# Performance work log

Measured on AMD Instinct MI355X. Metric: run time of the kernel, lower is better.

## Reference

```python
import jax, jax.numpy as jnp
import numpy as np

PLACEHOLDER = -1
B, S, V = 128, 8, 32000  # batch, spec tokens per request, vocab
T = B * S


def setup_inputs() -> dict:
    key = jax.random.key(0)
    ks = jax.random.split(key, 8)
    target_logits = jax.random.normal(ks[0], (T, V), dtype=jnp.float32)
    dp = jax.random.uniform(ks[1], (T, V), dtype=jnp.float32)
    draft_probs = dp / jnp.sum(dp, axis=-1, keepdims=True)  # valid prob dist per token
    draft_token_ids = jax.random.randint(ks[2], (T,), 0, V, dtype=jnp.int32)
    bonus_token_ids = jax.random.randint(ks[3], (B,), 0, V, dtype=jnp.int32)
    temperature = 0.5 + jax.random.uniform(ks[4], (B,), dtype=jnp.float32)  # >0 => all random
    uniform_probs = jax.random.uniform(ks[5], (T,), dtype=jnp.float32)
    # q ~ Exponential(1), as torch's q.exponential_()
    u = jax.random.uniform(ks[6], (B, V), dtype=jnp.float32, minval=1e-10, maxval=1.0)
    q = -jnp.log(u)
    cu_num_draft_tokens = (jnp.arange(B, dtype=jnp.int32) + 1) * S
    return {
        'target_logits': target_logits,
        'draft_probs': draft_probs,
        'draft_token_ids': draft_token_ids,
        'bonus_token_ids': bonus_token_ids,
        'temperature': temperature,
        'uniform_probs': uniform_probs,
        'q': q,
        'cu_num_draft_tokens': cu_num_draft_tokens,
    }


def reference(target_logits, draft_probs, draft_token_ids, bonus_token_ids,
              temperature, uniform_probs, q, cu_num_draft_tokens):
    # compute_probs: softmax of logits / per-token expanded temperature
    temp_tok = jnp.repeat(temperature, S)  # [T]
    target_probs = jax.nn.softmax(target_logits / temp_tok[:, None], axis=-1)  # [T, V]

    tok = jnp.arange(T)
    req = tok // S  # request index per token (uniform raggedness)

    # accept/reject: target_prob/draft_prob >= u  (guard draft_prob > 0)
    p_tgt = target_probs[tok, draft_token_ids]  # [T]
    p_drf = draft_probs[tok, draft_token_ids]   # [T]
    accept = (p_drf > 0) & (p_tgt >= uniform_probs * p_drf)  # [T]

    # recovered tokens: argmax(max(p_tgt - p_drf, 0) / q) over vocab (Gumbel-max trick)
    resid = jnp.maximum(target_probs - draft_probs, 0.0)  # [T, V]
    recovered = jnp.argmax(resid / q[req], axis=-1).astype(jnp.int32)  # [T]

    # sequential accept until first rejection, then placeholder; bonus if all accepted
    accept_b = accept.reshape(B, S)
    alive = jnp.concatenate(
        [jnp.ones((B, 1), dtype=bool),
         jnp.cumprod(accept_b[:, :-1].astype(jnp.int32), axis=1).astype(bool)],
        axis=1)  # alive[b, p] = all accepts before pos p
    tok_out = jnp.where(accept_b, draft_token_ids.reshape(B, S), recovered.reshape(B, S))
    main = jnp.where(alive, tok_out, PLACEHOLDER)  # [B, S]
    all_acc = jnp.all(accept_b, axis=1)
    bonus_col = jnp.where(all_acc, bonus_token_ids, PLACEHOLDER)  # [B]
    output_token_ids = jnp.concatenate([main, bonus_col[:, None]], axis=1)  # [B, S+1]
    return output_token_ids
```

## Files before the change

kernel.cpp:

```cpp
#include <hip/hip_runtime.h>


constexpr int PLACEHOLDER = -1;
constexpr int B = 128;
constexpr int S = 8;
constexpr int V = 32000;
constexpr int T = B * S;
constexpr int NV4 = V / 4;
constexpr int CHUNKS = 4;
constexpr int CV4 = NV4 / CHUNKS;
constexpr int K2T = 512;

extern "C" __device__ float __builtin_amdgcn_exp2f(float);
extern "C" __device__ float __builtin_amdgcn_rcpf(float);

__global__ __launch_bounds__(512)
void k1_sum(const float* __restrict__ logits,
            const float* __restrict__ dprobs,
            const int*   __restrict__ draft_ids,
            const float* __restrict__ temperature,
            const float* __restrict__ uniform_probs,
            float* __restrict__ w_D,
            int*   __restrict__ w_acc)
{
    const int t   = blockIdx.x;
    const int tid = threadIdx.x, lane = tid & 63, wid = tid >> 6;
    __shared__ float s_red[8];

    const float c = 1.4426950408889634f / temperature[t >> 3];
    const float4* lrow = (const float4*)(logits + (size_t)t * V);

    int dt = 0; float l_d = 0.f, d_d = 0.f, u = 0.f;
    if (tid == 0) {
        dt  = draft_ids[t];
        l_d = logits[(size_t)t * V + dt];
        d_d = dprobs[(size_t)t * V + dt];
        u   = uniform_probs[t];
    }

    float lsum = 0.f;
    #pragma unroll 4
    for (int j = 0; j < 16; ++j) {
        const int i4 = j * 512 + tid;
        if (i4 < NV4) {
            const float4 v = lrow[i4];
            lsum += (__builtin_amdgcn_exp2f(v.x * c) +
                     __builtin_amdgcn_exp2f(v.y * c)) +
                    (__builtin_amdgcn_exp2f(v.z * c) +
                     __builtin_amdgcn_exp2f(v.w * c));
        }
    }
    #pragma unroll
    for (int off = 32; off >= 1; off >>= 1)
        lsum += __shfl_xor(lsum, off, 64);
    if (lane == 0) s_red[wid] = lsum;
    __syncthreads();
    if (tid == 0) {
        const float D = ((s_red[0] + s_red[1]) + (s_red[2] + s_red[3])) +
                        ((s_red[4] + s_red[5]) + (s_red[6] + s_red[7]));
        w_D[t] = D;
        const float e_d = __builtin_amdgcn_exp2f(l_d * c);
        w_acc[t] = (d_d > 0.f) && (e_d >= u * d_d * D);
    }
}

__global__ __launch_bounds__(K2T)
void k2_arg(const float* __restrict__ logits,
            const float* __restrict__ dprobs,
            const float* __restrict__ q,
            const float* __restrict__ temperature,
            const float* __restrict__ w_D,
            const int*   __restrict__ w_acc,
            float* __restrict__ w_bv,
            int*   __restrict__ w_bi)
{
    const int bid = blockIdx.x;
    const int b = bid >> 2, k = bid & 3;
    const int tid = threadIdx.x, lane = tid & 63, wid = tid >> 6;
    __shared__ float s_val[8];
    __shared__ int   s_idx[8];
    __shared__ int   s_needp;

    if (tid == 0) {
        int np = S;
        #pragma unroll
        for (int p = S - 1; p >= 0; --p)
            if (!w_acc[b * S + p]) np = p;
        s_needp = np;
    }
    __syncthreads();
    const int need_p = s_needp;
    if (need_p >= S) return;

    const int   t = b * S + need_p;
    const float c = 1.4426950408889634f / temperature[b];
    const float D = w_D[t];

    const float4* lrow = (const float4*)(logits + (size_t)t * V) + k * CV4;
    const float4* drow = (const float4*)(dprobs + (size_t)t * V) + k * CV4;
    const float4* qrow = (const float4*)(q      + (size_t)b * V) + k * CV4;

    float4 lv[4], dv[4], qv[4];
    #pragma unroll
    for (int j = 0; j < 4; ++j) {
        const int i = j * K2T + tid;
        if (i < CV4) lv[j] = lrow[i];
    }
    #pragma unroll
    for (int j = 0; j < 4; ++j) {
        const int i = j * K2T + tid;
        if (i < CV4) dv[j] = drow[i];
    }
    #pragma unroll
    for (int j = 0; j < 4; ++j) {
        const int i = j * K2T + tid;
        if (i < CV4) qv[j] = qrow[i];
    }

    float bestv = -__builtin_inff();
    int   besti = 0x7fffffff;

#define RS_COMP(LC, DC, QC, GIDX)                                          \
    {                                                                      \
        const float e  = __builtin_amdgcn_exp2f((LC) * c);                 \
        const float rq = __builtin_amdgcn_rcpf(QC);                        \
        const float r  = fmaf(-((DC) * rq), D, e * rq);                    \
        if (r > bestv) { bestv = r; besti = (GIDX); }                      \
    }

    #pragma unroll
    for (int j = 0; j < 4; ++j) {
        const int i = j * K2T + tid;
        if (i < CV4) {
            const int base = (k * CV4 + i) * 4;
            RS_COMP(lv[j].x, dv[j].x, qv[j].x, base + 0)
            RS_COMP(lv[j].y, dv[j].y, qv[j].y, base + 1)
            RS_COMP(lv[j].z, dv[j].z, qv[j].z, base + 2)
            RS_COMP(lv[j].w, dv[j].w, qv[j].w, base + 3)
        }
    }
#undef RS_COMP

    #pragma unroll
    for (int off = 32; off >= 1; off >>= 1) {
        const float ov = __shfl_xor(bestv, off, 64);
        const int   oi = __shfl_xor(besti, off, 64);
        if (ov > bestv || (ov == bestv && oi < besti)) { bestv = ov; besti = oi; }
    }
    if (lane == 0) { s_val[wid] = bestv; s_idx[wid] = besti; }
    __syncthreads();
    if (tid == 0) {
        float bv = s_val[0]; int bi = s_idx[0];
        #pragma unroll
        for (int w = 1; w < 8; ++w) {
            const float ov = s_val[w]; const int oi = s_idx[w];
            if (ov > bv || (ov == bv && oi < bi)) { bv = ov; bi = oi; }
        }
        w_bv[bid] = bv;
        w_bi[bid] = bi;
    }
}

__global__ __launch_bounds__(128)
void k3_fin(const int*   __restrict__ w_acc,
            const int*   __restrict__ draft_ids,
            const int*   __restrict__ bonus_ids,
            const float* __restrict__ w_bv,
            const int*   __restrict__ w_bi,
            int* __restrict__ out)
{
    const int b = threadIdx.x;
    if (b >= B) return;
    int np = S;
    #pragma unroll
    for (int p = S - 1; p >= 0; --p)
        if (!w_acc[b * S + p]) np = p;

    int rec = PLACEHOLDER;
    if (np < S) {
        float bv = -__builtin_inff(); int bi = 0x7fffffff;
        #pragma unroll
        for (int kk = 0; kk < CHUNKS; ++kk) {
            const float ov = w_bv[b * CHUNKS + kk];
            const int   oi = w_bi[b * CHUNKS + kk];
            if (ov > bv || (ov == bv && oi < bi)) { bv = ov; bi = oi; }
        }
        rec = bi;
    }

    #pragma unroll
    for (int p = 0; p < S; ++p) {
        int tok = PLACEHOLDER;
        if (p < np)       tok = draft_ids[b * S + p];
        else if (p == np) tok = rec;
        out[b * (S + 1) + p] = tok;
    }
    out[b * (S + 1) + S] = (np == S) ? bonus_ids[b] : PLACEHOLDER;
}

extern "C" void kernel_launch(void* const* d_in, const int* in_sizes, int n_in,
                              void* d_out, int out_size, void* d_ws, size_t ws_size,
                              hipStream_t stream) {
    const float* logits      = (const float*)d_in[0];
    const float* dprobs      = (const float*)d_in[1];
    const int*   draft_ids   = (const int*)d_in[2];
    const int*   bonus_ids   = (const int*)d_in[3];
    const float* temperature = (const float*)d_in[4];
    const float* uniform     = (const float*)d_in[5];
    const float* q           = (const float*)d_in[6];

    int* out = (int*)d_out;
    float* w_D   = (float*)d_ws;
    int*   w_acc = (int*)(w_D + T);
    float* w_bv  = (float*)(w_acc + T);
    int*   w_bi  = (int*)(w_bv + B * CHUNKS);

    k1_sum<<<T, 512, 0, stream>>>(logits, dprobs, draft_ids, temperature,
                                  uniform, w_D, w_acc);
    k2_arg<<<B * CHUNKS, K2T, 0, stream>>>(logits, dprobs, q, temperature,
                                           w_D, w_acc, w_bv, w_bi);
    k3_fin<<<1, 128, 0, stream>>>(w_acc, draft_ids, bonus_ids, w_bv, w_bi, out);
}
```

Measured before the change: 37.81 us.

## Fuse final output kernel into argmax kernel via atomic max and last-block finalize

Removes the third kernel by having each argmax chunk block atomically merge a packed (ordered-float value, inverted index) key into a per-request 64-bit slot. A per-request counter picks the last finishing block, which writes the output row. Requests whose drafts are all accepted write their row directly. This saves a kernel launch and a small serial tail, but adds a hipMemsetAsync on the workspace plus atomic traffic.

After: 41.76 us. 10.4% more time.

```diff
diff --git a/kernel.cpp b/kernel.cpp
--- a/kernel.cpp
+++ b/kernel.cpp
@@ -64,6 +64,11 @@
     }
 }
 
+__device__ __forceinline__ unsigned int enc_f32(float f) {
+    const unsigned int s = __float_as_uint(f);
+    return ((int)s >= 0) ? (s | 0x80000000u) : ~s;
+}
+
 __global__ __launch_bounds__(K2T)
 void k2_arg(const float* __restrict__ logits,
             const float* __restrict__ dprobs,
@@ -71,8 +76,11 @@
             const float* __restrict__ temperature,
             const float* __restrict__ w_D,
             const int*   __restrict__ w_acc,
-            float* __restrict__ w_bv,
-            int*   __restrict__ w_bi)
+            const int*   __restrict__ draft_ids,
+            const int*   __restrict__ bonus_ids,
+            unsigned long long* __restrict__ w_best,
+            int* __restrict__ w_cnt,
+            int* __restrict__ out)
 {
     const int bid = blockIdx.x;
     const int b = bid >> 2, k = bid & 3;
@@ -90,7 +98,15 @@
     }
     __syncthreads();
     const int need_p = s_needp;
-    if (need_p >= S) return;
+    if (need_p >= S) {
+        if (k == 0 && tid == 0) {
+            #pragma unroll
+            for (int p = 0; p < S; ++p)
+                out[b * (S + 1) + p] = draft_ids[b * S + p];
+            out[b * (S + 1) + S] = bonus_ids[b];
+        }
+        return;
+    }
 
     const int   t = b * S + need_p;
     const float c = 1.4426950408889634f / temperature[b];
@@ -156,46 +172,29 @@
             const float ov = s_val[w]; const int oi = s_idx[w];
             if (ov > bv || (ov == bv && oi < bi)) { bv = ov; bi = oi; }
         }
-        w_bv[bid] = bv;
-        w_bi[bid] = bi;
-    }
-}
-
-__global__ __launch_bounds__(128)
-void k3_fin(const int*   __restrict__ w_acc,
-            const int*   __restrict__ draft_ids,
-            const int*   __restrict__ bonus_ids,
-            const float* __restrict__ w_bv,
-            const int*   __restrict__ w_bi,
-            int* __restrict__ out)
-{
-    const int b = threadIdx.x;
-    if (b >= B) return;
-    int np = S;
-    #pragma unroll
-    for (int p = S - 1; p >= 0; --p)
-        if (!w_acc[b * S + p]) np = p;
-
-    int rec = PLACEHOLDER;
-    if (np < S) {
-        float bv = -__builtin_inff(); int bi = 0x7fffffff;
-        #pragma unroll
-        for (int kk = 0; kk < CHUNKS; ++kk) {
-            const float ov = w_bv[b * CHUNKS + kk];
-            const int   oi = w_bi[b * CHUNKS + kk];
-            if (ov > bv || (ov == bv && oi < bi)) { bv = ov; bi = oi; }
-        }
-        rec = bi;
-    }
-
-    #pragma unroll
-    for (int p = 0; p < S; ++p) {
-        int tok = PLACEHOLDER;
-        if (p < np)       tok = draft_ids[b * S + p];
-        else if (p == np) tok = rec;
-        out[b * (S + 1) + p] = tok;
-    }
-    out[b * (S + 1) + S] = (np == S) ? bonus_ids[b] : PLACEHOLDER;
+        const unsigned long long packed =
+            ((unsigned long long)enc_f32(bv) << 32) |
+            (unsigned int)(~(unsigned int)bi);
+        __hip_atomic_fetch_max(&w_best[b], packed, __ATOMIC_RELAXED,
+                               __HIP_MEMORY_SCOPE_AGENT);
+        asm volatile("s_waitcnt vmcnt(0)" ::: "memory");
+        const int old = __hip_atomic_fetch_add(&w_cnt[b], 1, __ATOMIC_RELAXED,
+                                               __HIP_MEMORY_SCOPE_AGENT);
+        if (old == CHUNKS - 1) {
+            const unsigned long long fin =
+                __hip_atomic_load(&w_best[b], __ATOMIC_RELAXED,
+                                  __HIP_MEMORY_SCOPE_AGENT);
+            const int rec = (int)(~(unsigned int)(fin & 0xFFFFFFFFull));
+            #pragma unroll
+            for (int p = 0; p < S; ++p) {
+                int tok = PLACEHOLDER;
+                if (p < need_p)       tok = draft_ids[b * S + p];
+                else if (p == need_p) tok = rec;
+                out[b * (S + 1) + p] = tok;
+            }
+            out[b * (S + 1) + S] = PLACEHOLDER;
+        }
+    }
 }
 
 extern "C" void kernel_launch(void* const* d_in, const int* in_sizes, int n_in,
@@ -212,12 +211,15 @@
     int* out = (int*)d_out;
     float* w_D   = (float*)d_ws;
     int*   w_acc = (int*)(w_D + T);
-    float* w_bv  = (float*)(w_acc + T);
-    int*   w_bi  = (int*)(w_bv + B * CHUNKS);
+    unsigned long long* w_best = (unsigned long long*)(w_acc + T);
+    int*   w_cnt = (int*)(w_best + B);
+
+    hipMemsetAsync(w_best, 0, B * sizeof(unsigned long long) + B * sizeof(int),
+                   stream);
 
     k1_sum<<<T, 512, 0, stream>>>(logits, dprobs, draft_ids, temperature,
                                   uniform, w_D, w_acc);
     k2_arg<<<B * CHUNKS, K2T, 0, stream>>>(logits, dprobs, q, temperature,
-                                           w_D, w_acc, w_bv, w_bi);
-    k3_fin<<<1, 128, 0, stream>>>(w_acc, draft_ids, bonus_ids, w_bv, w_bi, out);
-}
+                                           w_D, w_acc, draft_ids, bonus_ids,
+                                           w_best, w_cnt, out);
+}
```
